# Kernel tuning notes

Hardware: AMD Instinct MI355X
Metric: run time of the kernel (lower is better)

Reference implementation:

```python
import jax, jax.numpy as jnp
import numpy as np

N_HEADS = 16
D_MODEL = 1024
D_HEAD = D_MODEL // N_HEADS


def setup_inputs() -> dict:
    key = jax.random.key(0)
    k1, k2, k3, k4, k5 = jax.random.split(key, 5)
    B, S = 4, 2048
    scale = 1.0 / np.sqrt(D_MODEL)
    return {
        "x": jax.random.normal(k1, (B, S, D_MODEL), dtype=jnp.float32),
        "W_in": jax.random.normal(k2, (3 * D_MODEL, D_MODEL), dtype=jnp.float32) * scale,
        "b_in": jax.random.normal(k3, (3 * D_MODEL,), dtype=jnp.float32) * 0.02,
        "W_out": jax.random.normal(k4, (D_MODEL, D_MODEL), dtype=jnp.float32) * scale,
        "b_out": jax.random.normal(k5, (D_MODEL,), dtype=jnp.float32) * 0.02,
        "causal_mask": 1,
    }


def reference(x, W_in, b_in, W_out, b_out, causal_mask):
    b, s, d = x.shape
    # in_proj: torch Linear -> x @ W.T + b, then chunk into q,k,v
    qkv = jnp.einsum("bsd,ed->bse", x, W_in) + b_in
    q, k, v = jnp.split(qkv, 3, axis=-1)
    # [b, s, h, dh] -> [b, h, s, dh]
    q = q.reshape(b, s, N_HEADS, D_HEAD).transpose(0, 2, 1, 3)
    k = k.reshape(b, s, N_HEADS, D_HEAD).transpose(0, 2, 1, 3)
    v = v.reshape(b, s, N_HEADS, D_HEAD).transpose(0, 2, 1, 3)
    # scores [b, h, s, s]
    qk = jnp.einsum("bhqd,bhkd->bhqk", q, k)
    if causal_mask:
        mask = jnp.triu(jnp.ones((s, s), dtype=bool), k=1)
        qk = jnp.where(mask, -jnp.inf, qk)
    qk = qk / jnp.sqrt(jnp.float32(D_HEAD))
    attn = jax.nn.softmax(qk, axis=-1)
    out = jnp.einsum("bhqk,bhkd->bhqd", attn, v)  # [b, h, s, dh]
    out = out.transpose(0, 2, 1, 3).reshape(b, s, d)
    return jnp.einsum("bsd,ed->bse", out, W_out) + b_out
```

## Files before the change

### kernel.cpp

```cpp
#include <hip/hip_runtime.h>
#include <hip/hip_bf16.h>
#include <cstdint>
#include <cstddef>

typedef short bf16x8 __attribute__((ext_vector_type(8)));
typedef float f32x4 __attribute__((ext_vector_type(4)));

#define SEQ 2048
#define NH 16
#define DH 64
#define DM 1024

typedef __attribute__((address_space(1))) const void gvoid_t;
typedef __attribute__((address_space(3))) void lvoid_t;

__device__ __forceinline__ unsigned short f2bf(float f) {
  union { float f; unsigned int u; } v; v.f = f;
  return (unsigned short)((v.u + 0x7FFFu + ((v.u >> 16) & 1u)) >> 16);
}

__global__ void __launch_bounds__(256) k_cvt3(const float* __restrict__ x,
                                              const float* __restrict__ wi,
                                              const float* __restrict__ wo,
                                              unsigned short* __restrict__ xb,
                                              unsigned short* __restrict__ wib,
                                              unsigned short* __restrict__ wob) {
  int bidx = blockIdx.x;
  const float* src; unsigned short* dst; int base;
  if (bidx < 8192)       { src = x;  dst = xb;  base = bidx; }
  else if (bidx < 11264) { src = wi; dst = wib; base = bidx - 8192; }
  else                   { src = wo; dst = wob; base = bidx - 11264; }
  int i = (base * 256 + threadIdx.x) * 4;
  float4 v = *(const float4*)(src + i);
  ushort4 o;
  o.x = f2bf(v.x); o.y = f2bf(v.y); o.z = f2bf(v.z); o.w = f2bf(v.w);
  *(ushort4*)(dst + i) = o;
}

#define LDS_T 16384

__device__ __forceinline__ void barx() {
  asm volatile("" ::: "memory");
  __builtin_amdgcn_s_barrier();
  asm volatile("" ::: "memory");
}
#define LGKM0() asm volatile("s_waitcnt lgkmcnt(0)" ::: "memory")
#define VMC4()  asm volatile("s_waitcnt vmcnt(4)" ::: "memory")

__device__ __forceinline__ void stage_half(const unsigned short* __restrict__ G,
                                           int row0, int kt, unsigned short* lds,
                                           int Rhalf, int rstat, int cOff, int wave) {
#pragma unroll
  for (int pc = 0; pc < 2; ++pc) {
    const int R = Rhalf + pc * 64;
    __builtin_amdgcn_global_load_lds(
        (gvoid_t*)(G + (size_t)(row0 + R + rstat) * DM + kt * 64 + cOff),
        (lvoid_t*)(lds + (R + wave * 8) * 64), 16, 0, 0);
  }
}

__device__ __forceinline__ void lda8(const unsigned short* lds, int rb, int l16,
                                     int sw0, int sw1, bf16x8 (&a)[8]) {
#pragma unroll
  for (int f = 0; f < 4; ++f) {
    const unsigned short* p = lds + (rb + f * 16 + l16) * 64;
    a[f * 2 + 0] = *(const bf16x8*)(p + sw0);
    a[f * 2 + 1] = *(const bf16x8*)(p + sw1);
  }
}

__device__ __forceinline__ void ldb4(const unsigned short* lds, int rb, int l16,
                                     int sw0, int sw1, bf16x8 (&b)[4]) {
#pragma unroll
  for (int g = 0; g < 2; ++g) {
    const unsigned short* p = lds + (rb + g * 16 + l16) * 64;
    b[g * 2 + 0] = *(const bf16x8*)(p + sw0);
    b[g * 2 + 1] = *(const bf16x8*)(p + sw1);
  }
}

template <int MQ, int NQ>
__device__ __forceinline__ void mfma_quad(const bf16x8 (&a)[8], const bf16x8 (&b)[4],
                                          f32x4 (&acc)[8][4]) {
  __builtin_amdgcn_s_setprio(1);
#pragma unroll
  for (int f = 0; f < 4; ++f)
#pragma unroll
    for (int g = 0; g < 2; ++g) {
      f32x4 c = acc[MQ * 4 + f][NQ * 2 + g];
      c = __builtin_amdgcn_mfma_f32_16x16x32_bf16(a[f * 2 + 0], b[g * 2 + 0], c, 0, 0, 0);
      c = __builtin_amdgcn_mfma_f32_16x16x32_bf16(a[f * 2 + 1], b[g * 2 + 1], c, 0, 0, 0);
      acc[MQ * 4 + f][NQ * 2 + g] = c;
    }
  __builtin_amdgcn_s_setprio(0);
}

__device__ __forceinline__ void gemm256(const unsigned short* __restrict__ A,
                                        const unsigned short* __restrict__ Bt,
                                        unsigned short* lA, unsigned short* lB,
                                        int m0, int n0, f32x4 (&acc)[8][4]) {
  const int t = threadIdx.x;
  const int wave = t >> 6, lane = t & 63, quad = lane >> 4, l16 = lane & 15;
  const int wm = wave >> 2, wn = wave & 3;
  const int rstat = t >> 3;
  const int cOff = ((t & 7) ^ (rstat & 7)) * 8;
  const int sw0 = (quad ^ (l16 & 7)) * 8;
  const int sw1 = ((quad ^ 4) ^ (l16 & 7)) * 8;
  const int arb0 = wm * 64, arb1 = 128 + wm * 64;
  const int brb0 = wn * 32, brb1 = 128 + wn * 32;
  const int NT = DM / 64;

  bf16x8 af[8], b0[4], b1[4];

  stage_half(A,  m0, 0, lA, 0,   rstat, cOff, wave);
  stage_half(Bt, n0, 0, lB, 0,   rstat, cOff, wave);
  stage_half(A,  m0, 0, lA, 128, rstat, cOff, wave);
  stage_half(Bt, n0, 0, lB, 128, rstat, cOff, wave);
  stage_half(A,  m0, 1, lA + LDS_T, 0,   rstat, cOff, wave);
  stage_half(Bt, n0, 1, lB + LDS_T, 128, rstat, cOff, wave);
  VMC4();
  barx();

  for (int t0 = 0; t0 < NT; t0 += 2) {
    const int t2 = (t0 + 2 < NT) ? t0 + 2 : NT - 1;
    const int t3 = (t0 + 3 < NT) ? t0 + 3 : NT - 1;
    lda8(lA, arb0, l16, sw0, sw1, af);
    ldb4(lB, brb0, l16, sw0, sw1, b0);
    stage_half(A, m0, t0 + 1, lA + LDS_T, 128, rstat, cOff, wave);
    barx(); LGKM0();
    mfma_quad<0, 0>(af, b0, acc);
    barx();
    ldb4(lB, brb1, l16, sw0, sw1, b1);
    stage_half(Bt, n0, t0 + 1, lB + LDS_T, 0, rstat, cOff, wave);
    barx(); LGKM0();
    mfma_quad<0, 1>(af, b1, acc);
    barx();
    lda8(lA, arb1, l16, sw0, sw1, af);
    stage_half(A, m0, t2, lA, 0, rstat, cOff, wave);
    barx(); LGKM0();
    mfma_quad<1, 1>(af, b1, acc);
    barx();
    stage_half(Bt, n0, t2, lB, 128, rstat, cOff, wave);
    VMC4();
    barx(); LGKM0();
    mfma_quad<1, 0>(af, b0, acc);
    barx();
    lda8(lA + LDS_T, arb0, l16, sw0, sw1, af);
    ldb4(lB + LDS_T, brb0, l16, sw0, sw1, b0);
    stage_half(A, m0, t2, lA, 128, rstat, cOff, wave);
    barx(); LGKM0();
    mfma_quad<0, 0>(af, b0, acc);
    barx();
    ldb4(lB + LDS_T, brb1, l16, sw0, sw1, b1);
    stage_half(Bt, n0, t2, lB, 0, rstat, cOff, wave);
    barx(); LGKM0();
    mfma_quad<0, 1>(af, b1, acc);
    barx();
    lda8(lA + LDS_T, arb1, l16, sw0, sw1, af);
    stage_half(A, m0, t3, lA + LDS_T, 0, rstat, cOff, wave);
    barx(); LGKM0();
    mfma_quad<1, 1>(af, b1, acc);
    barx();
    stage_half(Bt, n0, t3, lB + LDS_T, 128, rstat, cOff, wave);
    VMC4();
    barx(); LGKM0();
    mfma_quad<1, 0>(af, b0, acc);
    barx();
  }
}

__global__ void __launch_bounds__(512, 2) k_gemm_qkv(
    const unsigned short* __restrict__ X,
    const unsigned short* __restrict__ Wi,
    const float* __restrict__ bias,
    unsigned short* __restrict__ Qo,
    unsigned short* __restrict__ Ko,
    unsigned short* __restrict__ Vto) {
  __shared__ unsigned short lA[2 * LDS_T];
  __shared__ unsigned short lB[2 * LDS_T];
  const int t = threadIdx.x;
  const int wave = t >> 6, lane = t & 63, quad = lane >> 4, l16 = lane & 15;
  const int wm = wave >> 2, wn = wave & 3;
  const int nwg = 32 * 12;
  const int bid = blockIdx.x;
  const int swz = (bid & 7) * (nwg / 8) + (bid >> 3);
  const int m0 = (swz / 12) * 256, n0 = (swz % 12) * 256;

  f32x4 acc[8][4];
  f32x4 zf = {0.f, 0.f, 0.f, 0.f};
#pragma unroll
  for (int i = 0; i < 8; ++i)
#pragma unroll
    for (int j = 0; j < 4; ++j) acc[i][j] = zf;

  gemm256(X, Wi, lA, lB, m0, n0, acc);

  const float SCALE = 0.18033688011112042f;
  const int sel = n0 >> 10;
#pragma unroll
  for (int nf = 0; nf < 4; ++nf) {
    const int gcol = n0 + (nf >> 1) * 128 + wn * 32 + (nf & 1) * 16 + l16;
    const float bv = bias[gcol];
    const int c = gcol & 1023;
    const int hh = c >> 6, dh = c & 63;
    if (sel == 0) {
#pragma unroll
      for (int mf = 0; mf < 8; ++mf) {
        const int grow = m0 + (mf >> 2) * 128 + wm * 64 + (mf & 3) * 16 + quad * 4;
        const int bb = grow >> 11, sb = grow & 2047;
        unsigned short* qp = Qo + ((size_t)(bb * NH + hh) * SEQ + sb) * DH + dh;
#pragma unroll
        for (int r = 0; r < 4; ++r)
          qp[(size_t)r * DH] = f2bf((acc[mf][nf][r] + bv) * SCALE);
      }
    } else if (sel == 1) {
#pragma unroll
      for (int mf = 0; mf < 8; ++mf) {
        const int grow = m0 + (mf >> 2) * 128 + wm * 64 + (mf & 3) * 16 + quad * 4;
        const int bb = grow >> 11, sb = grow & 2047;
        unsigned short* kp = Ko + ((size_t)(bb * NH + hh) * SEQ + sb) * DH + dh;
#pragma unroll
        for (int r = 0; r < 4; ++r)
          kp[(size_t)r * DH] = f2bf(acc[mf][nf][r] + bv);
      }
    } else {
#pragma unroll
      for (int mf = 0; mf < 8; ++mf) {
        const int grow = m0 + (mf >> 2) * 128 + wm * 64 + (mf & 3) * 16 + quad * 4;
        const int bb = grow >> 11, sb = grow & 2047;
        ushort4 pk;
        pk.x = f2bf(acc[mf][nf][0] + bv);
        pk.y = f2bf(acc[mf][nf][1] + bv);
        pk.z = f2bf(acc[mf][nf][2] + bv);
        pk.w = f2bf(acc[mf][nf][3] + bv);
        *(ushort4*)(&Vto[((size_t)(bb * NH + hh) * DH + dh) * SEQ + sb]) = pk;
      }
    }
  }
}

#define ASTR 72

__global__ void __launch_bounds__(256, 4) k_attn(
    const unsigned short* __restrict__ Q,
    const unsigned short* __restrict__ K,
    const unsigned short* __restrict__ Vt,
    unsigned short* __restrict__ Ao,
    const int* __restrict__ causal_p) {
  __shared__ unsigned short lK[64 * 64];
  __shared__ unsigned short lV[64 * 64];
  __shared__ unsigned short lP[2][4][16 * ASTR];

  const int t = threadIdx.x;
  const int wave = t >> 6, lane = t & 63, quad = lane >> 4, l16 = lane & 15;
  const int x = blockIdx.x, h = blockIdx.y, b = blockIdx.z;
  const int qtA = x, qtB = 31 - x;
  const int bh = b * NH + h;
  const int causal = causal_p[0];
  const int ktA = causal ? qtA : 31;
  const int ktB = causal ? qtB : 31;
  const int q0A = qtA * 64, q0B = qtB * 64;

  const unsigned short* Qb = Q + (size_t)bh * SEQ * DH;
  const unsigned short* Kb = K + (size_t)bh * SEQ * DH;
  const unsigned short* Vb = Vt + (size_t)bh * DH * SEQ;

  bf16x8 qA0 = *(const bf16x8*)(&Qb[(q0A + wave * 16 + l16) * DH + quad * 8]);
  bf16x8 qA1 = *(const bf16x8*)(&Qb[(q0A + wave * 16 + l16) * DH + 32 + quad * 8]);
  bf16x8 qB0 = *(const bf16x8*)(&Qb[(q0B + wave * 16 + l16) * DH + quad * 8]);
  bf16x8 qB1 = *(const bf16x8*)(&Qb[(q0B + wave * 16 + l16) * DH + 32 + quad * 8]);

  f32x4 zf = {0.f, 0.f, 0.f, 0.f};
  f32x4 oA[4], oB[4];
  for (int i = 0; i < 4; ++i) { oA[i] = zf; oB[i] = zf; }
  f32x4 lacA = zf, lacB = zf;

  bf16x8 ones;
#pragma unroll
  for (int i = 0; i < 8; ++i) ones[i] = (short)0x3F80;

  unsigned short* lPa = &lP[0][wave][0];
  unsigned short* lPb = &lP[1][wave][0];

  const int i0 = t, i1 = 256 + t;
  const int rr0 = i0 >> 3, cc0 = ((i0 & 7) ^ (rr0 & 7)) * 8;
  const int rr1 = i1 >> 3, cc1 = ((i1 & 7) ^ (rr1 & 7)) * 8;
  const int kof0 = rr0 * DH + cc0, kof1 = rr1 * DH + cc1;
  const int vof0 = rr0 * SEQ + cc0, vof1 = rr1 * SEQ + cc1;
  const int rbase = l16 * 64;
  const int sw0 = ((quad ^ (l16 & 7)) * 8);
  const int sw1 = (((quad ^ 4) ^ (l16 & 7)) * 8);

  for (int kt = 0; kt <= ktB; ++kt) {
    const int k0 = kt * 64;
    const bool doA = (kt <= ktA);

    __syncthreads();
    __builtin_amdgcn_global_load_lds((gvoid_t*)(Kb + (size_t)k0 * DH + kof0),
                                     (lvoid_t*)&lK[wave * 512], 16, 0, 0);
    __builtin_amdgcn_global_load_lds((gvoid_t*)(Kb + (size_t)k0 * DH + kof1),
                                     (lvoid_t*)&lK[wave * 512 + 2048], 16, 0, 0);
    __builtin_amdgcn_global_load_lds((gvoid_t*)(Vb + k0 + vof0),
                                     (lvoid_t*)&lV[wave * 512], 16, 0, 0);
    __builtin_amdgcn_global_load_lds((gvoid_t*)(Vb + k0 + vof1),
                                     (lvoid_t*)&lV[wave * 512 + 2048], 16, 0, 0);
    __syncthreads();

    f32x4 sA[4], sB[4];
#pragma unroll
    for (int nt = 0; nt < 4; ++nt) {
      bf16x8 kf0 = *(const bf16x8*)(&lK[nt * 1024 + rbase + sw0]);
      bf16x8 kf1 = *(const bf16x8*)(&lK[nt * 1024 + rbase + sw1]);
      f32x4 zb = zf;
      zb = __builtin_amdgcn_mfma_f32_16x16x32_bf16(qB0, kf0, zb, 0, 0, 0);
      zb = __builtin_amdgcn_mfma_f32_16x16x32_bf16(qB1, kf1, zb, 0, 0, 0);
      sB[nt] = zb;
      if (doA) {
        f32x4 za = zf;
        za = __builtin_amdgcn_mfma_f32_16x16x32_bf16(qA0, kf0, za, 0, 0, 0);
        za = __builtin_amdgcn_mfma_f32_16x16x32_bf16(qA1, kf1, za, 0, 0, 0);
        sA[nt] = za;
      }
    }

    if (causal && kt == qtB) {
#pragma unroll
      for (int nt = 0; nt < 4; ++nt) {
        int kcol = k0 + nt * 16 + l16;
#pragma unroll
        for (int r = 0; r < 4; ++r)
          if (kcol > q0B + wave * 16 + quad * 4 + r) sB[nt][r] = -1e30f;
      }
    }
    if (causal && doA && kt == qtA) {
#pragma unroll
      for (int nt = 0; nt < 4; ++nt) {
        int kcol = k0 + nt * 16 + l16;
#pragma unroll
        for (int r = 0; r < 4; ++r)
          if (kcol > q0A + wave * 16 + quad * 4 + r) sA[nt][r] = -1e30f;
      }
    }

#pragma unroll
    for (int nt = 0; nt < 4; ++nt)
#pragma unroll
      for (int r = 0; r < 4; ++r)
        lPb[(quad * 4 + r) * ASTR + nt * 16 + l16] =
            f2bf(__builtin_amdgcn_exp2f(sB[nt][r]));
    if (doA) {
#pragma unroll
      for (int nt = 0; nt < 4; ++nt)
#pragma unroll
        for (int r = 0; r < 4; ++r)
          lPa[(quad * 4 + r) * ASTR + nt * 16 + l16] =
              f2bf(__builtin_amdgcn_exp2f(sA[nt][r]));
    }

    asm volatile("s_waitcnt lgkmcnt(0)" ::: "memory");

    bf16x8 pB0 = *(const bf16x8*)(&lPb[l16 * ASTR + quad * 8]);
    bf16x8 pB1 = *(const bf16x8*)(&lPb[l16 * ASTR + 32 + quad * 8]);
    bf16x8 pA0 = pB0, pA1 = pB1;
    if (doA) {
      pA0 = *(const bf16x8*)(&lPa[l16 * ASTR + quad * 8]);
      pA1 = *(const bf16x8*)(&lPa[l16 * ASTR + 32 + quad * 8]);
    }

    lacB = __builtin_amdgcn_mfma_f32_16x16x32_bf16(pB0, ones, lacB, 0, 0, 0);
    lacB = __builtin_amdgcn_mfma_f32_16x16x32_bf16(pB1, ones, lacB, 0, 0, 0);
    if (doA) {
      lacA = __builtin_amdgcn_mfma_f32_16x16x32_bf16(pA0, ones, lacA, 0, 0, 0);
      lacA = __builtin_amdgcn_mfma_f32_16x16x32_bf16(pA1, ones, lacA, 0, 0, 0);
    }

#pragma unroll
    for (int nt = 0; nt < 4; ++nt) {
      bf16x8 vf0 = *(const bf16x8*)(&lV[nt * 1024 + rbase + sw0]);
      bf16x8 vf1 = *(const bf16x8*)(&lV[nt * 1024 + rbase + sw1]);
      oB[nt] = __builtin_amdgcn_mfma_f32_16x16x32_bf16(pB0, vf0, oB[nt], 0, 0, 0);
      oB[nt] = __builtin_amdgcn_mfma_f32_16x16x32_bf16(pB1, vf1, oB[nt], 0, 0, 0);
      if (doA) {
        oA[nt] = __builtin_amdgcn_mfma_f32_16x16x32_bf16(pA0, vf0, oA[nt], 0, 0, 0);
        oA[nt] = __builtin_amdgcn_mfma_f32_16x16x32_bf16(pA1, vf1, oA[nt], 0, 0, 0);
      }
    }
  }

#pragma unroll
  for (int r = 0; r < 4; ++r) {
    float invB = 1.0f / lacB[r];
    float invA = 1.0f / lacA[r];
#pragma unroll
    for (int nt = 0; nt < 4; ++nt) {
      int dh = nt * 16 + l16;
      int qgB = q0B + wave * 16 + quad * 4 + r;
      Ao[(size_t)(b * SEQ + qgB) * DM + h * DH + dh] = f2bf(oB[nt][r] * invB);
      int qgA = q0A + wave * 16 + quad * 4 + r;
      Ao[(size_t)(b * SEQ + qgA) * DM + h * DH + dh] = f2bf(oA[nt][r] * invA);
    }
  }
}

__global__ void __launch_bounds__(512, 2) k_gemm_out(
    const unsigned short* __restrict__ Ai,
    const unsigned short* __restrict__ Wo,
    const float* __restrict__ bias,
    float* __restrict__ C) {
  __shared__ unsigned short lA[2 * LDS_T];
  __shared__ unsigned short lB[2 * LDS_T];
  const int t = threadIdx.x;
  const int wave = t >> 6, lane = t & 63, quad = lane >> 4, l16 = lane & 15;
  const int wm = wave >> 2, wn = wave & 3;
  const int bid = blockIdx.x;
  const int swz = (bid & 7) * 16 + (bid >> 3);
  const int m0 = (swz >> 2) * 256, n0 = (swz & 3) * 256;

  f32x4 acc[8][4];
  f32x4 zf = {0.f, 0.f, 0.f, 0.f};
#pragma unroll
  for (int i = 0; i < 8; ++i)
#pragma unroll
    for (int j = 0; j < 4; ++j) acc[i][j] = zf;

  gemm256(Ai, Wo, lA, lB, m0, n0, acc);

#pragma unroll
  for (int nf = 0; nf < 4; ++nf) {
    const int gcol = n0 + (nf >> 1) * 128 + wn * 32 + (nf & 1) * 16 + l16;
    const float bv = bias[gcol];
#pragma unroll
    for (int mf = 0; mf < 8; ++mf) {
      const int grow = m0 + (mf >> 2) * 128 + wm * 64 + (mf & 3) * 16 + quad * 4;
#pragma unroll
      for (int r = 0; r < 4; ++r)
        C[(size_t)(grow + r) * DM + gcol] = acc[mf][nf][r] + bv;
    }
  }
}

extern "C" void kernel_launch(void* const* d_in, const int* in_sizes, int n_in,
                              void* d_out, int out_size, void* d_ws, size_t ws_size,
                              hipStream_t stream) {
  (void)in_sizes; (void)n_in; (void)out_size; (void)ws_size;
  const float* x     = (const float*)d_in[0];
  const float* W_in  = (const float*)d_in[1];
  const float* b_in  = (const float*)d_in[2];
  const float* W_out = (const float*)d_in[3];
  const float* b_out = (const float*)d_in[4];
  const int* causal  = (const int*)d_in[5];
  float* out = (float*)d_out;
  char* ws = (char*)d_ws;

  unsigned short* xb  = (unsigned short*)(ws + 0);
  unsigned short* Aob = (unsigned short*)(ws + 0);
  unsigned short* Wib = (unsigned short*)(ws + (size_t)(16 << 20));
  unsigned short* Wob = (unsigned short*)(ws + (size_t)(22 << 20));
  unsigned short* Qb  = (unsigned short*)(ws + (size_t)(24 << 20));
  unsigned short* Kb  = (unsigned short*)(ws + (size_t)(40 << 20));
  unsigned short* Vtb = (unsigned short*)(ws + (size_t)(56 << 20));

  k_cvt3<<<12288, 256, 0, stream>>>(x, W_in, W_out, xb, Wib, Wob);
  k_gemm_qkv<<<384, 512, 0, stream>>>(xb, Wib, b_in, Qb, Kb, Vtb);
  k_attn<<<dim3(16, 16, 4), 256, 0, stream>>>(Qb, Kb, Vtb, Aob, causal);
  k_gemm_out<<<128, 512, 0, stream>>>(Aob, Wob, b_out, out);
}
```

Before: 262.1 us.

## Retile output GEMM to 128x128 tiles and remap attention blocks per XCD

The output projection GEMM now uses 128x128 tiles with 256 threads and 512 blocks instead of 128 large 256x256 blocks, so more CUs are filled. The new tile loop is single-buffered, with synchronization around each K step. It gives up the double-buffered pipelining of the shared gemm256 path. The attention kernel switches to a 1D grid with an XCD-aware remap so that blocks sharing a head land on the same XCD, improving L2 reuse of K/V.

```diff
diff --git a/kernel.cpp b/kernel.cpp
--- a/kernel.cpp
+++ b/kernel.cpp
@@ -18,6 +18,14 @@
   union { float f; unsigned int u; } v; v.f = f;
   return (unsigned short)((v.u + 0x7FFFu + ((v.u >> 16) & 1u)) >> 16);
 }
+
+__device__ __forceinline__ void barx() {
+  asm volatile("" ::: "memory");
+  __builtin_amdgcn_s_barrier();
+  asm volatile("" ::: "memory");
+}
+#define LGKM0() asm volatile("s_waitcnt lgkmcnt(0)" ::: "memory")
+#define VMC4()  asm volatile("s_waitcnt vmcnt(4)" ::: "memory")
 
 __global__ void __launch_bounds__(256) k_cvt3(const float* __restrict__ x,
                                               const float* __restrict__ wi,
@@ -39,14 +47,6 @@
 
 #define LDS_T 16384
 
-__device__ __forceinline__ void barx() {
-  asm volatile("" ::: "memory");
-  __builtin_amdgcn_s_barrier();
-  asm volatile("" ::: "memory");
-}
-#define LGKM0() asm volatile("s_waitcnt lgkmcnt(0)" ::: "memory")
-#define VMC4()  asm volatile("s_waitcnt vmcnt(4)" ::: "memory")
-
 __device__ __forceinline__ void stage_half(const unsigned short* __restrict__ G,
                                            int row0, int kt, unsigned short* lds,
                                            int Rhalf, int rstat, int cOff, int wave) {
@@ -101,11 +101,12 @@
                                         int m0, int n0, f32x4 (&acc)[8][4]) {
   const int t = threadIdx.x;
   const int wave = t >> 6, lane = t & 63, quad = lane >> 4, l16 = lane & 15;
-  const int wm = wave >> 2, wn = wave & 3;
+  (void)lane;
   const int rstat = t >> 3;
   const int cOff = ((t & 7) ^ (rstat & 7)) * 8;
   const int sw0 = (quad ^ (l16 & 7)) * 8;
   const int sw1 = ((quad ^ 4) ^ (l16 & 7)) * 8;
+  const int wm = wave >> 2, wn = wave & 3;
   const int arb0 = wm * 64, arb1 = 128 + wm * 64;
   const int brb0 = wn * 32, brb1 = 128 + wn * 32;
   const int NT = DM / 64;
@@ -180,6 +181,7 @@
   __shared__ unsigned short lB[2 * LDS_T];
   const int t = threadIdx.x;
   const int wave = t >> 6, lane = t & 63, quad = lane >> 4, l16 = lane & 15;
+  (void)lane;
   const int wm = wave >> 2, wn = wave & 3;
   const int nwg = 32 * 12;
   const int bid = blockIdx.x;
@@ -253,7 +255,10 @@
 
   const int t = threadIdx.x;
   const int wave = t >> 6, lane = t & 63, quad = lane >> 4, l16 = lane & 15;
-  const int x = blockIdx.x, h = blockIdx.y, b = blockIdx.z;
+  const int id = blockIdx.x;
+  const int cxcd = id & 7, w = id >> 3;
+  const int x = w & 15, g = (w >> 4) * 8 + cxcd;
+  const int h = g & 15, b = g >> 4;
   const int qtA = x, qtB = 31 - x;
   const int bh = b * NH + h;
   const int causal = causal_p[0];
@@ -402,39 +407,86 @@
   }
 }
 
-__global__ void __launch_bounds__(512, 2) k_gemm_out(
+__device__ __forceinline__ void gemm_tile_bt(const unsigned short* __restrict__ A,
+                                             const unsigned short* __restrict__ Bt,
+                                             unsigned short* lA, unsigned short* lB,
+                                             int m0, int n0, f32x4 (&acc)[4][4]) {
+  const int t = threadIdx.x;
+  const int wave = t >> 6, lane = t & 63, quad = lane >> 4, l16 = lane & 15;
+  (void)lane;
+  const int mh = (wave >> 1) * 64, nh = (wave & 1) * 64;
+  int row_[4], c_[4];
+#pragma unroll
+  for (int r = 0; r < 4; ++r) {
+    int i = r * 256 + t;
+    row_[r] = i >> 3;
+    c_[r] = ((i & 7) ^ ((i >> 3) & 7)) * 8;
+  }
+  const int sw0 = ((quad) ^ (l16 & 7)) * 8;
+  const int sw1 = ((quad ^ 4) ^ (l16 & 7)) * 8;
+  for (int k0 = 0; k0 < DM; k0 += 64) {
+    __syncthreads();
+#pragma unroll
+    for (int r = 0; r < 4; ++r) {
+      __builtin_amdgcn_global_load_lds((gvoid_t*)&A[(size_t)(m0 + row_[r]) * DM + k0 + c_[r]],
+                                       (lvoid_t*)&lA[(r * 4 + wave) * 512], 16, 0, 0);
+      __builtin_amdgcn_global_load_lds((gvoid_t*)&Bt[(size_t)(n0 + row_[r]) * DM + k0 + c_[r]],
+                                       (lvoid_t*)&lB[(r * 4 + wave) * 512], 16, 0, 0);
+    }
+    __syncthreads();
+    bf16x8 af[4], bfr[4];
+#pragma unroll
+    for (int i = 0; i < 4; ++i)
+      af[i] = *(const bf16x8*)(&lA[(mh + i * 16 + l16) * 64 + sw0]);
+#pragma unroll
+    for (int i = 0; i < 4; ++i)
+      bfr[i] = *(const bf16x8*)(&lB[(nh + i * 16 + l16) * 64 + sw0]);
+#pragma unroll
+    for (int mt = 0; mt < 4; ++mt)
+#pragma unroll
+      for (int nt = 0; nt < 4; ++nt)
+        acc[mt][nt] = __builtin_amdgcn_mfma_f32_16x16x32_bf16(af[mt], bfr[nt], acc[mt][nt], 0, 0, 0);
+#pragma unroll
+    for (int i = 0; i < 4; ++i)
+      af[i] = *(const bf16x8*)(&lA[(mh + i * 16 + l16) * 64 + sw1]);
+#pragma unroll
+    for (int i = 0; i < 4; ++i)
+      bfr[i] = *(const bf16x8*)(&lB[(nh + i * 16 + l16) * 64 + sw1]);
+#pragma unroll
+    for (int mt = 0; mt < 4; ++mt)
+#pragma unroll
+      for (int nt = 0; nt < 4; ++nt)
+        acc[mt][nt] = __builtin_amdgcn_mfma_f32_16x16x32_bf16(af[mt], bfr[nt], acc[mt][nt], 0, 0, 0);
+  }
+}
+
+__global__ void __launch_bounds__(256, 2) k_gemm_out(
     const unsigned short* __restrict__ Ai,
     const unsigned short* __restrict__ Wo,
     const float* __restrict__ bias,
     float* __restrict__ C) {
-  __shared__ unsigned short lA[2 * LDS_T];
-  __shared__ unsigned short lB[2 * LDS_T];
+  __shared__ unsigned short lA[128 * 64];
+  __shared__ unsigned short lB[128 * 64];
   const int t = threadIdx.x;
   const int wave = t >> 6, lane = t & 63, quad = lane >> 4, l16 = lane & 15;
-  const int wm = wave >> 2, wn = wave & 3;
-  const int bid = blockIdx.x;
-  const int swz = (bid & 7) * 16 + (bid >> 3);
-  const int m0 = (swz >> 2) * 256, n0 = (swz & 3) * 256;
-
-  f32x4 acc[8][4];
+  (void)lane;
+  const int m0 = blockIdx.x * 128, n0 = blockIdx.y * 128;
+  f32x4 acc[4][4];
   f32x4 zf = {0.f, 0.f, 0.f, 0.f};
-#pragma unroll
-  for (int i = 0; i < 8; ++i)
-#pragma unroll
+  for (int i = 0; i < 4; ++i)
     for (int j = 0; j < 4; ++j) acc[i][j] = zf;
-
-  gemm256(Ai, Wo, lA, lB, m0, n0, acc);
-
-#pragma unroll
-  for (int nf = 0; nf < 4; ++nf) {
-    const int gcol = n0 + (nf >> 1) * 128 + wn * 32 + (nf & 1) * 16 + l16;
-    const float bv = bias[gcol];
-#pragma unroll
-    for (int mf = 0; mf < 8; ++mf) {
-      const int grow = m0 + (mf >> 2) * 128 + wm * 64 + (mf & 3) * 16 + quad * 4;
+  gemm_tile_bt(Ai, Wo, lA, lB, m0, n0, acc);
+  const int mh = (wave >> 1) * 64, nh = (wave & 1) * 64;
+#pragma unroll
+  for (int nt = 0; nt < 4; ++nt) {
+    int gcol = n0 + nh + nt * 16 + l16;
+    float bv = bias[gcol];
+#pragma unroll
+    for (int mt = 0; mt < 4; ++mt) {
+      int rowbase = m0 + mh + mt * 16 + quad * 4;
 #pragma unroll
       for (int r = 0; r < 4; ++r)
-        C[(size_t)(grow + r) * DM + gcol] = acc[mf][nf][r] + bv;
+        C[(size_t)(rowbase + r) * DM + gcol] = acc[mt][nt][r] + bv;
     }
   }
 }
@@ -462,6 +514,6 @@
 
   k_cvt3<<<12288, 256, 0, stream>>>(x, W_in, W_out, xb, Wib, Wob);
   k_gemm_qkv<<<384, 512, 0, stream>>>(xb, Wib, b_in, Qb, Kb, Vtb);
-  k_attn<<<dim3(16, 16, 4), 256, 0, stream>>>(Qb, Kb, Vtb, Aob, causal);
-  k_gemm_out<<<128, 512, 0, stream>>>(Aob, Wob, b_out, out);
-}
+  k_attn<<<1024, 256, 0, stream>>>(Qb, Kb, Vtb, Aob, causal);
+  k_gemm_out<<<dim3(64, 8), 256, 0, stream>>>(Aob, Wob, b_out, out);
+}
```

Result: faster. 251.5 us (-4.0%).
